# Kernel optimization log

Hardware: AMD Instinct MI355X
Metric: run time of the kernel (lower is better)

## Reference

```python
import jax, jax.numpy as jnp
import numpy as np

B, S, D = 2, 2048, 1024
H, DK, DV = 16, 64, 64
N_WINDOW = 256
LN_EPS = 1e-5


def setup_inputs() -> dict:
    key = jax.random.key(0)
    ks = jax.random.split(key, 8)
    sc = 0.02
    return {
        "Q": jax.random.normal(ks[0], (B, S, D), jnp.float32),
        "K": jax.random.normal(ks[1], (B, S, D), jnp.float32),
        "V": jax.random.normal(ks[2], (B, S, D), jnp.float32),
        "Wq": jax.random.normal(ks[3], (D, H * DK), jnp.float32) * sc,
        "bq": jnp.zeros((H * DK,), jnp.float32),
        "Wk": jax.random.normal(ks[4], (D, H * DK), jnp.float32) * sc,
        "bk": jnp.zeros((H * DK,), jnp.float32),
        "Wv": jax.random.normal(ks[5], (D, H * DV), jnp.float32) * sc,
        "bv": jnp.zeros((H * DV,), jnp.float32),
        "Wo": jax.random.normal(ks[6], (H * DV, D), jnp.float32) * sc,
        "bo": jnp.zeros((D,), jnp.float32),
        "gamma": jnp.ones((D,), jnp.float32),
        "beta": jnp.zeros((D,), jnp.float32),
    }


def reference(Q, K, V, Wq, bq, Wk, bk, Wv, bv, Wo, bo, gamma, beta):
    b, s, _ = Q.shape
    # QKV projections -> [b, s, h, d]
    q = (Q @ Wq + bq).reshape(b, s, H, DK)
    k = (K @ Wk + bk).reshape(b, s, H, DK)
    v = (V @ Wv + bv).reshape(b, s, H, DV)
    # scores [b, h, i, j]
    scores = jnp.einsum("bihd,bjhd->bhij", q, k) / np.sqrt(DK).astype(np.float32)
    # sliding-window band mask |i - j| < N_WINDOW (mask=True path)
    idx = jnp.arange(s)
    band = jnp.abs(idx[:, None] - idx[None, :]) < N_WINDOW  # [s, s]
    scores = jnp.where(band[None, None], scores, -jnp.inf)
    attn = jax.nn.softmax(scores, axis=-1)
    ctx = jnp.einsum("bhij,bjhd->bihd", attn, v).reshape(b, s, H * DV)
    out = ctx @ Wo + bo
    # residual + LayerNorm over last dim
    x = out + Q
    mu = jnp.mean(x, axis=-1, keepdims=True)
    var = jnp.mean(jnp.square(x - mu), axis=-1, keepdims=True)
    y = (x - mu) * jax.lax.rsqrt(var + LN_EPS) * gamma + beta
    return y, attn
```

## Files before the change

### kernel.cpp

```cpp
#include <hip/hip_runtime.h>
#include <hip/hip_bf16.h>

#define BB 2
#define SS 2048
#define HH 16
#define LN_EPS 1e-5f
#define LOG2E 1.44269504088896f

typedef __attribute__((ext_vector_type(8))) short short8;
typedef __attribute__((ext_vector_type(4))) float floatx4;

#define EXP2F(x) __builtin_amdgcn_exp2f(x)
#define GLOAD16(g, l) __builtin_amdgcn_global_load_lds( \
    (const __attribute__((address_space(1))) void*)(g), \
    (__attribute__((address_space(3))) void*)(l), 16, 0, 0)

__device__ __forceinline__ ushort f2b(float f) {
    union { float f; unsigned u; } x; x.f = f;
    unsigned u = x.u;
    return (ushort)((u + 0x7FFFu + ((u >> 16) & 1u)) >> 16);
}
__device__ __forceinline__ float b2f(ushort u) {
    union { unsigned u; float f; } x; x.u = ((unsigned)u) << 16;
    return x.f;
}

__global__ __launch_bounds__(256) void prep(
    const float* __restrict__ Q, const float* __restrict__ K, const float* __restrict__ V,
    const float* __restrict__ W0, const float* __restrict__ W1,
    const float* __restrict__ W2, const float* __restrict__ W3,
    ushort* __restrict__ Xq, ushort* __restrict__ Xk, ushort* __restrict__ Xv,
    ushort* __restrict__ T0, ushort* __restrict__ T1,
    ushort* __restrict__ T2, ushort* __restrict__ T3)
{
    __shared__ float ts[32][33];
    const int z = blockIdx.z;
    if (z < 3) {
        const float* X = z == 0 ? Q : z == 1 ? K : V;
        ushort* Y = z == 0 ? Xq : z == 1 ? Xk : Xv;
        const size_t i = ((size_t)blockIdx.x * 256 + threadIdx.x) * 8;
        float4 a = *(const float4*)&X[i];
        float4 b = *(const float4*)&X[i + 4];
        short8 o;
        o[0] = (short)f2b(a.x); o[1] = (short)f2b(a.y); o[2] = (short)f2b(a.z); o[3] = (short)f2b(a.w);
        o[4] = (short)f2b(b.x); o[5] = (short)f2b(b.y); o[6] = (short)f2b(b.z); o[7] = (short)f2b(b.w);
        *(short8*)&Y[i] = o;
    } else {
        if (blockIdx.x >= 1024) return;
        const int zz = z - 3;
        const float* W = zz == 0 ? W0 : zz == 1 ? W1 : zz == 2 ? W2 : W3;
        ushort* T = zz == 0 ? T0 : zz == 1 ? T1 : zz == 2 ? T2 : T3;
        const float scale = (zz == 0) ? 0.125f : 1.0f;
        const int k0 = (blockIdx.x >> 5) * 32, n0 = (blockIdx.x & 31) * 32;
        const int r = threadIdx.x >> 3, c4 = (threadIdx.x & 7) * 4;
        float4 v = *(const float4*)&W[(size_t)(k0 + r) * 1024 + n0 + c4];
        ts[r][c4 + 0] = v.x; ts[r][c4 + 1] = v.y; ts[r][c4 + 2] = v.z; ts[r][c4 + 3] = v.w;
        __syncthreads();
        ushort4 o;
        o.x = f2b(ts[c4 + 0][r] * scale); o.y = f2b(ts[c4 + 1][r] * scale);
        o.z = f2b(ts[c4 + 2][r] * scale); o.w = f2b(ts[c4 + 3][r] * scale);
        *(ushort4*)&T[(size_t)(n0 + r) * 1024 + k0 + c4] = o;
    }
}

template<int NB>
__device__ __forceinline__ void gemm_body(
    const ushort* __restrict__ Ab, const ushort* __restrict__ Bt,
    const float* __restrict__ bias, float bscale,
    float* Cf, ushort* Cb, int m0, int n0)
{
    __shared__ ushort As[2][128 * 32];
    __shared__ ushort Bs[2][NB * 32 * 32];
    const int t = threadIdx.x;
    const int l = t & 63;
    const int w = t >> 6;
    const int wm = w >> 1, wn = w & 1;

    floatx4 acc[4][NB] = {};

    const int i0c = w * 64 + l;
    const int r0 = i0c >> 2, c0 = i0c & 3;
    const int i1c = 256 + i0c;
    const int r1 = i1c >> 2, c1 = i1c & 3;

    const ushort* gA0 = &Ab[(size_t)(m0 + r0) * 1024 + c0 * 8];
    const ushort* gA1 = &Ab[(size_t)(m0 + r1) * 1024 + c1 * 8];
    const ushort* gB0 = &Bt[(size_t)(n0 + r0) * 1024 + c0 * 8];
    const ushort* gB1 = &Bt[(size_t)(n0 + ((NB == 4) ? r1 : r0)) * 1024 + ((NB == 4) ? c1 : c0) * 8];

    const int d0 = (w * 64) * 16;
    const int d1 = (256 + w * 64) * 16;

    GLOAD16(gA0, (char*)As[0] + d0);
    GLOAD16(gA1, (char*)As[0] + d1);
    GLOAD16(gB0, (char*)Bs[0] + d0);
    if (NB == 4) GLOAD16(gB1, (char*)Bs[0] + d1);
    __syncthreads();

    int cur = 0;
    for (int k0 = 0; k0 < 1024; k0 += 32) {
        if (k0 + 32 < 1024) {
            GLOAD16(gA0 + k0 + 32, (char*)As[cur ^ 1] + d0);
            GLOAD16(gA1 + k0 + 32, (char*)As[cur ^ 1] + d1);
            GLOAD16(gB0 + k0 + 32, (char*)Bs[cur ^ 1] + d0);
            if (NB == 4) GLOAD16(gB1 + k0 + 32, (char*)Bs[cur ^ 1] + d1);
        }
        short8 af[4], bf[NB];
#pragma unroll
        for (int m = 0; m < 4; ++m)
            af[m] = *(const short8*)&As[cur][(wm * 64 + m * 16 + (l & 15)) * 32 + (l >> 4) * 8];
#pragma unroll
        for (int n = 0; n < NB; ++n)
            bf[n] = *(const short8*)&Bs[cur][(wn * (NB * 16) + n * 16 + (l & 15)) * 32 + (l >> 4) * 8];
#pragma unroll
        for (int m = 0; m < 4; ++m)
#pragma unroll
            for (int n = 0; n < NB; ++n)
                acc[m][n] = __builtin_amdgcn_mfma_f32_16x16x32_bf16(af[m], bf[n], acc[m][n], 0, 0, 0);
        __syncthreads();
        cur ^= 1;
    }

    const int cr = (l >> 4) * 4;
    const int cc = l & 15;
#pragma unroll
    for (int n = 0; n < NB; ++n) {
        int col = n0 + wn * (NB * 16) + n * 16 + cc;
        float bv = bias[col] * bscale;
#pragma unroll
        for (int m = 0; m < 4; ++m) {
            int row = m0 + wm * 64 + m * 16 + cr;
#pragma unroll
            for (int j = 0; j < 4; ++j) {
                float v = acc[m][n][j] + bv;
                if (Cf) Cf[(size_t)(row + j) * 1024 + col] = v;
                else    Cb[(size_t)(row + j) * 1024 + col] = f2b(v);
            }
        }
    }
}

__global__ __launch_bounds__(256) void gemm_qkv(
    const ushort* __restrict__ Xq, const ushort* __restrict__ Xk, const ushort* __restrict__ Xv,
    const ushort* __restrict__ Wqt, const ushort* __restrict__ Wkt, const ushort* __restrict__ Wvt,
    const float* __restrict__ bq, const float* __restrict__ bk, const float* __restrict__ bv,
    ushort* __restrict__ qp, ushort* __restrict__ kp, ushort* __restrict__ vp)
{
    const int z = blockIdx.z;
    const ushort* A = z == 0 ? Xq : z == 1 ? Xk : Xv;
    const ushort* Bt = z == 0 ? Wqt : z == 1 ? Wkt : Wvt;
    const float* bias = z == 0 ? bq : z == 1 ? bk : bv;
    ushort* C = z == 0 ? qp : z == 1 ? kp : vp;
    float bscale = (z == 0) ? 0.125f : 1.0f;
    int bid = blockIdx.x + (blockIdx.y << 3);
    int xcd = bid & 7, idx = bid >> 3;
    int m0 = (xcd * 4 + (idx & 3)) * 128;
    int n0 = (idx >> 2) * 128;
    gemm_body<4>(A, Bt, bias, bscale, nullptr, C, m0, n0);
}

__global__ __launch_bounds__(256) void gemm_obf(
    const ushort* __restrict__ ctxb, const ushort* __restrict__ Wot,
    const float* __restrict__ bo, float* __restrict__ op)
{
    int bid = blockIdx.x + (blockIdx.y << 3);
    int xcd = bid & 7, idx = bid >> 3;
    int m0 = (xcd * 4 + (idx & 3)) * 128;
    int n0 = (idx >> 2) * 64;
    gemm_body<2>(ctxb, Wot, bo, 1.0f, op, nullptr, m0, n0);
}

__global__ __launch_bounds__(256, 4) void attn_mfma(
    const ushort* __restrict__ qb, const ushort* __restrict__ kb, const ushort* __restrict__ vb,
    float* __restrict__ attn, ushort* __restrict__ ctxb)
{
    __shared__ alignas(16) ushort Vt[2][64 * 72];
    __shared__ alignas(16) ushort Pl[4][16 * 72];

    const int qblk = blockIdx.x, h = blockIdx.y, b = blockIdx.z;
    const int i0 = qblk * 64;
    const int t = threadIdx.x;
    const int w = t >> 6, l = t & 63;
    const int g = l >> 4, c = l & 15;
    const int ibase = i0 + w * 16;

    const int jstart = max(0, i0 - 256);
    const int jend = min(SS, i0 + 64 + 256);

    const size_t qoff = (size_t)(b * SS + ibase + c) * 1024 + h * 64 + g * 8;
    short8 aq0 = *(const short8*)&qb[qoff];
    short8 aq1 = *(const short8*)&qb[qoff + 32];

    {
        float* ab = attn + (size_t)(b * HH + h) * SS * SS;
        const floatx4 z4 = {0.f, 0.f, 0.f, 0.f};
        const int g16 = t >> 4, c16 = t & 15;
#pragma unroll
        for (int rr = 0; rr < 4; ++rr) {
            float* rp = ab + (size_t)(i0 + g16 + rr * 16) * SS;
            for (int x = c16 * 4; x < jstart; x += 64)
                __builtin_nontemporal_store(z4, (floatx4*)&rp[x]);
            for (int x = jend + c16 * 4; x < SS; x += 64)
                __builtin_nontemporal_store(z4, (floatx4*)&rp[x]);
        }
    }

    const int vj0 = (t & 31) * 2, vd0 = (t >> 5) * 8;
    const ushort* Kbh = &kb[(size_t)(b * SS) * 1024 + h * 64];

    float m[4] = {-3e38f, -3e38f, -3e38f, -3e38f};
    float ll[4] = {0.f, 0.f, 0.f, 0.f};

    for (int jt = jstart; jt < jend; jt += 64) {
        const ushort* kt = Kbh + (size_t)jt * 1024;
        floatx4 s[4] = {};
#pragma unroll
        for (int u = 0; u < 4; ++u) {
            short8 b0 = *(const short8*)&kt[(size_t)(u * 16 + c) * 1024 + g * 8];
            short8 b1 = *(const short8*)&kt[(size_t)(u * 16 + c) * 1024 + 32 + g * 8];
            s[u] = __builtin_amdgcn_mfma_f32_16x16x32_bf16(aq0, b0, s[u], 0, 0, 0);
            s[u] = __builtin_amdgcn_mfma_f32_16x16x32_bf16(aq1, b1, s[u], 0, 0, 0);
        }
        const bool full = (jt >= ibase - 240) && (jt <= ibase + 192);
#pragma unroll
        for (int r = 0; r < 4; ++r) {
            float v0 = s[0][r] * LOG2E, v1 = s[1][r] * LOG2E,
                  v2 = s[2][r] * LOG2E, v3 = s[3][r] * LOG2E;
            if (!full) {
                const int i = ibase + g * 4 + r;
                const int j0 = jt + c;
                if ((unsigned)(i - j0 + 255) >= 511u)        v0 = -3e38f;
                if ((unsigned)(i - (j0 + 16) + 255) >= 511u) v1 = -3e38f;
                if ((unsigned)(i - (j0 + 32) + 255) >= 511u) v2 = -3e38f;
                if ((unsigned)(i - (j0 + 48) + 255) >= 511u) v3 = -3e38f;
            }
            float tmax = fmaxf(fmaxf(v0, v1), fmaxf(v2, v3));
            float mn = fmaxf(m[r], tmax);
            float sc_ = EXP2F(m[r] - mn);
            float add = EXP2F(v0 - mn) + EXP2F(v1 - mn)
                      + EXP2F(v2 - mn) + EXP2F(v3 - mn);
            ll[r] = ll[r] * sc_ + add;
            m[r] = mn;
        }
    }

    float M[4], invL[4];
#pragma unroll
    for (int r = 0; r < 4; ++r) {
        float mm = m[r];
        mm = fmaxf(mm, __shfl_xor(mm, 1));
        mm = fmaxf(mm, __shfl_xor(mm, 2));
        mm = fmaxf(mm, __shfl_xor(mm, 4));
        mm = fmaxf(mm, __shfl_xor(mm, 8));
        float la = ll[r] * EXP2F(m[r] - mm);
        la += __shfl_xor(la, 1);
        la += __shfl_xor(la, 2);
        la += __shfl_xor(la, 4);
        la += __shfl_xor(la, 8);
        M[r] = mm;
        invL[r] = 1.0f / la;
    }

    {
        const ushort* vr = &vb[(size_t)(b * SS + jstart + vj0) * 1024 + h * 64 + vd0];
        short8 v0 = *(const short8*)vr;
        short8 v1 = *(const short8*)(vr + 1024);
#pragma unroll
        for (int e = 0; e < 8; ++e) {
            ushort2 pr; pr.x = (ushort)v0[e]; pr.y = (ushort)v1[e];
            *(ushort2*)&Vt[0][(vd0 + e) * 72 + vj0] = pr;
        }
    }
    __syncthreads();

    floatx4 ctx[4] = {};
    int cur = 0;
    for (int jt = jstart; jt < jend; jt += 64) {
        const bool have = (jt + 64 < jend);
        short8 nv0, nv1;
        if (have) {
            const ushort* vr = &vb[(size_t)(b * SS + jt + 64 + vj0) * 1024 + h * 64 + vd0];
            nv0 = *(const short8*)vr;
            nv1 = *(const short8*)(vr + 1024);
        }
        const ushort* kt = Kbh + (size_t)jt * 1024;
        floatx4 s[4] = {};
#pragma unroll
        for (int u = 0; u < 4; ++u) {
            short8 b0 = *(const short8*)&kt[(size_t)(u * 16 + c) * 1024 + g * 8];
            short8 b1 = *(const short8*)&kt[(size_t)(u * 16 + c) * 1024 + 32 + g * 8];
            s[u] = __builtin_amdgcn_mfma_f32_16x16x32_bf16(aq0, b0, s[u], 0, 0, 0);
            s[u] = __builtin_amdgcn_mfma_f32_16x16x32_bf16(aq1, b1, s[u], 0, 0, 0);
        }
        const bool full = (jt >= ibase - 240) && (jt <= ibase + 192);
#pragma unroll
        for (int u = 0; u < 4; ++u) {
#pragma unroll
            for (int r = 0; r < 4; ++r) {
                float v = s[u][r] * LOG2E;
                if (!full) {
                    const int i = ibase + g * 4 + r;
                    const int j = jt + u * 16 + c;
                    if ((unsigned)(i - j + 255) >= 511u) v = -3e38f;
                }
                float p = EXP2F(v - M[r]) * invL[r];
                Pl[w][(g * 4 + r) * 72 + u * 16 + c] = f2b(p);
            }
        }
#pragma unroll
        for (int it = 0; it < 4; ++it) {
            const int row = it * 4 + g;
            ushort4 pw = *(const ushort4*)&Pl[w][row * 72 + c * 4];
            floatx4 o;
            o[0] = b2f(pw.x); o[1] = b2f(pw.y); o[2] = b2f(pw.z); o[3] = b2f(pw.w);
            __builtin_nontemporal_store(o,
                (floatx4*)&attn[(size_t)(b * HH + h) * SS * SS + (size_t)(ibase + row) * SS + jt + c * 4]);
        }
#pragma unroll
        for (int jc = 0; jc < 2; ++jc) {
            short8 pa = *(const short8*)&Pl[w][c * 72 + jc * 32 + g * 8];
#pragma unroll
            for (int ds = 0; ds < 4; ++ds) {
                short8 bv_ = *(const short8*)&Vt[cur][(ds * 16 + c) * 72 + jc * 32 + g * 8];
                ctx[ds] = __builtin_amdgcn_mfma_f32_16x16x32_bf16(pa, bv_, ctx[ds], 0, 0, 0);
            }
        }
        if (have) {
#pragma unroll
            for (int e = 0; e < 8; ++e) {
                ushort2 pr; pr.x = (ushort)nv0[e]; pr.y = (ushort)nv1[e];
                *(ushort2*)&Vt[cur ^ 1][(vd0 + e) * 72 + vj0] = pr;
            }
        }
        __syncthreads();
        cur ^= 1;
    }

#pragma unroll
    for (int ds = 0; ds < 4; ++ds)
#pragma unroll
        for (int r = 0; r < 4; ++r)
            ctxb[(size_t)(b * SS + ibase + g * 4 + r) * 1024 + h * 64 + ds * 16 + c] = f2b(ctx[ds][r]);
}

__global__ __launch_bounds__(256) void ln_kernel(
    const float* __restrict__ op, const float* __restrict__ Qin,
    const float* __restrict__ gamma, const float* __restrict__ beta,
    float* __restrict__ y)
{
    const int row = blockIdx.x;
    const int t = threadIdx.x;
    __shared__ float rs[4], rss[4];

    float4 o4 = *(const float4*)&op[(size_t)row * 1024 + t * 4];
    float4 q4 = *(const float4*)&Qin[(size_t)row * 1024 + t * 4];
    float x0 = o4.x + q4.x, x1 = o4.y + q4.y, x2 = o4.z + q4.z, x3 = o4.w + q4.w;
    float s = x0 + x1 + x2 + x3;
    float ss = x0 * x0 + x1 * x1 + x2 * x2 + x3 * x3;
#pragma unroll
    for (int off = 1; off < 64; off <<= 1) {
        s  += __shfl_xor(s, off, 64);
        ss += __shfl_xor(ss, off, 64);
    }
    int wid = t >> 6;
    if ((t & 63) == 0) { rs[wid] = s; rss[wid] = ss; }
    __syncthreads();
    s  = rs[0] + rs[1] + rs[2] + rs[3];
    ss = rss[0] + rss[1] + rss[2] + rss[3];
    float mu = s * (1.0f / 1024.0f);
    float var = ss * (1.0f / 1024.0f) - mu * mu;
    float rstd = rsqrtf(var + LN_EPS);
    float4 g4 = *(const float4*)&gamma[t * 4];
    float4 b4 = *(const float4*)&beta[t * 4];
    float4 o;
    o.x = (x0 - mu) * rstd * g4.x + b4.x;
    o.y = (x1 - mu) * rstd * g4.y + b4.y;
    o.z = (x2 - mu) * rstd * g4.z + b4.z;
    o.w = (x3 - mu) * rstd * g4.w + b4.w;
    *(float4*)&y[(size_t)row * 1024 + t * 4] = o;
}

extern "C" void kernel_launch(void* const* d_in, const int* in_sizes, int n_in,
                              void* d_out, int out_size, void* d_ws, size_t ws_size,
                              hipStream_t stream) {
    (void)in_sizes; (void)n_in; (void)out_size; (void)ws_size;
    const float* Q  = (const float*)d_in[0];
    const float* K  = (const float*)d_in[1];
    const float* V  = (const float*)d_in[2];
    const float* Wq = (const float*)d_in[3];
    const float* bq = (const float*)d_in[4];
    const float* Wk = (const float*)d_in[5];
    const float* bk = (const float*)d_in[6];
    const float* Wv = (const float*)d_in[7];
    const float* bv = (const float*)d_in[8];
    const float* Wo = (const float*)d_in[9];
    const float* bo = (const float*)d_in[10];
    const float* gamma = (const float*)d_in[11];
    const float* beta  = (const float*)d_in[12];

    float* y = (float*)d_out;
    float* attn = y + (size_t)BB * SS * 1024;

    char* base = (char*)d_ws;
    float*  op   = (float*)base;
    ushort* Xq   = (ushort*)base;
    ushort* Xk   = (ushort*)(base + (size_t)8 * 1048576);
    ushort* Xv   = (ushort*)(base + (size_t)16 * 1048576);
    ushort* ctxb = (ushort*)(base + (size_t)16 * 1048576);
    ushort* qbp  = (ushort*)(base + (size_t)24 * 1048576);
    ushort* kbp  = (ushort*)(base + (size_t)32 * 1048576);
    ushort* vbp  = (ushort*)(base + (size_t)40 * 1048576);
    ushort* Wqt  = (ushort*)(base + (size_t)48 * 1048576);
    ushort* Wkt  = (ushort*)(base + (size_t)50 * 1048576);
    ushort* Wvt  = (ushort*)(base + (size_t)52 * 1048576);
    ushort* Wot  = (ushort*)(base + (size_t)54 * 1048576);

    prep<<<dim3(2048, 1, 7), 256, 0, stream>>>(Q, K, V, Wq, Wk, Wv, Wo,
                                               Xq, Xk, Xv, Wqt, Wkt, Wvt, Wot);
    gemm_qkv<<<dim3(8, 32, 3), 256, 0, stream>>>(Xq, Xk, Xv, Wqt, Wkt, Wvt, bq, bk, bv, qbp, kbp, vbp);
    attn_mfma<<<dim3(SS / 64, HH, BB), 256, 0, stream>>>(qbp, kbp, vbp, attn, ctxb);
    gemm_obf<<<dim3(8, 64), 256, 0, stream>>>(ctxb, Wot, bo, op);
    ln_kernel<<<4096, 256, 0, stream>>>(op, Q, gamma, beta, y);
}
```

Measured before the change: 225.9 us.

## Overlap attention zero-fill stores with QKV and output GEMM main loops

Moves the zeroing of the out-of-band parts of the attention matrix out of the attention kernel and spreads it across the k-loop iterations of the QKV and output-projection GEMMs. Each GEMM block writes one 64x64 zero tile per iteration. The goal is to hide the large store traffic behind compute-bound MFMA work. The cost is extra bookkeeping and stores competing with the GEMM loads, plus a fixed tile enumeration that depends on exact grid sizes.

```diff
diff --git a/kernel.cpp b/kernel.cpp
--- a/kernel.cpp
+++ b/kernel.cpp
@@ -67,7 +67,8 @@
 __device__ __forceinline__ void gemm_body(
     const ushort* __restrict__ Ab, const ushort* __restrict__ Bt,
     const float* __restrict__ bias, float bscale,
-    float* Cf, ushort* Cb, int m0, int n0)
+    float* Cf, ushort* Cb, int m0, int n0,
+    float* __restrict__ attnf, int f_lo, int f_hi)
 {
     __shared__ ushort As[2][128 * 32];
     __shared__ ushort Bs[2][NB * 32 * 32];
@@ -90,6 +91,21 @@
 
     const int d0 = (w * 64) * 16;
     const int d1 = (256 + w * 64) * 16;
+
+    int fleft = f_hi - f_lo;
+    int fbh = 0, fq = 0, frr = 0;
+    if (fleft > 0) {
+        fbh = f_lo / 756;
+        int r = f_lo - fbh * 756;
+        while (true) {
+            int cnt = (fq > 4 ? fq - 4 : 0) + (fq < 27 ? 27 - fq : 0);
+            if (r < cnt) break;
+            r -= cnt; ++fq;
+        }
+        frr = r;
+    }
+    const int ftrow = t >> 2, ftc = (t & 3) * 16;
+    const floatx4 fz = {0.f, 0.f, 0.f, 0.f};
 
     GLOAD16(gA0, (char*)As[0] + d0);
     GLOAD16(gA1, (char*)As[0] + d1);
@@ -105,6 +121,19 @@
             GLOAD16(gB0 + k0 + 32, (char*)Bs[cur ^ 1] + d0);
             if (NB == 4) GLOAD16(gB1 + k0 + 32, (char*)Bs[cur ^ 1] + d1);
         }
+        if (fleft > 0) {
+            int L = fq > 4 ? fq - 4 : 0;
+            int col = (frr < L) ? frr * 64 : (fq * 64 + 320 + (frr - L) * 64);
+            float* fp = attnf + (size_t)fbh * ((size_t)SS * SS)
+                      + (size_t)(fq * 64 + ftrow) * SS + col + ftc;
+            __builtin_nontemporal_store(fz, (floatx4*)fp);
+            __builtin_nontemporal_store(fz, (floatx4*)(fp + 4));
+            __builtin_nontemporal_store(fz, (floatx4*)(fp + 8));
+            __builtin_nontemporal_store(fz, (floatx4*)(fp + 12));
+            --fleft; ++frr;
+            int cnt = L + (fq < 27 ? 27 - fq : 0);
+            if (frr >= cnt) { frr = 0; ++fq; if (fq == 32) { fq = 0; ++fbh; } }
+        }
         short8 af[4], bf[NB];
 #pragma unroll
         for (int m = 0; m < 4; ++m)
@@ -144,7 +173,8 @@
     const ushort* __restrict__ Xq, const ushort* __restrict__ Xk, const ushort* __restrict__ Xv,
     const ushort* __restrict__ Wqt, const ushort* __restrict__ Wkt, const ushort* __restrict__ Wvt,
     const float* __restrict__ bq, const float* __restrict__ bk, const float* __restrict__ bv,
-    ushort* __restrict__ qp, ushort* __restrict__ kp, ushort* __restrict__ vp)
+    ushort* __restrict__ qp, ushort* __restrict__ kp, ushort* __restrict__ vp,
+    float* __restrict__ attnf)
 {
     const int z = blockIdx.z;
     const ushort* A = z == 0 ? Xq : z == 1 ? Xk : Xv;
@@ -156,18 +186,22 @@
     int xcd = bid & 7, idx = bid >> 3;
     int m0 = (xcd * 4 + (idx & 3)) * 128;
     int n0 = (idx >> 2) * 128;
-    gemm_body<4>(A, Bt, bias, bscale, nullptr, C, m0, n0);
+    int k = bid + z * 256;
+    gemm_body<4>(A, Bt, bias, bscale, nullptr, C, m0, n0, attnf, k * 21, k * 21 + 21);
 }
 
 __global__ __launch_bounds__(256) void gemm_obf(
     const ushort* __restrict__ ctxb, const ushort* __restrict__ Wot,
-    const float* __restrict__ bo, float* __restrict__ op)
+    const float* __restrict__ bo, float* __restrict__ op,
+    float* __restrict__ attnf)
 {
     int bid = blockIdx.x + (blockIdx.y << 3);
     int xcd = bid & 7, idx = bid >> 3;
     int m0 = (xcd * 4 + (idx & 3)) * 128;
     int n0 = (idx >> 2) * 64;
-    gemm_body<2>(ctxb, Wot, bo, 1.0f, op, nullptr, m0, n0);
+    int lo = 16128 + bid * 16;
+    int hi = lo + 16; if (hi > 24192) hi = 24192; if (lo > 24192) lo = 24192;
+    gemm_body<2>(ctxb, Wot, bo, 1.0f, op, nullptr, m0, n0, attnf, lo, hi);
 }
 
 __global__ __launch_bounds__(256, 4) void attn_mfma(
@@ -190,20 +224,6 @@
     const size_t qoff = (size_t)(b * SS + ibase + c) * 1024 + h * 64 + g * 8;
     short8 aq0 = *(const short8*)&qb[qoff];
     short8 aq1 = *(const short8*)&qb[qoff + 32];
-
-    {
-        float* ab = attn + (size_t)(b * HH + h) * SS * SS;
-        const floatx4 z4 = {0.f, 0.f, 0.f, 0.f};
-        const int g16 = t >> 4, c16 = t & 15;
-#pragma unroll
-        for (int rr = 0; rr < 4; ++rr) {
-            float* rp = ab + (size_t)(i0 + g16 + rr * 16) * SS;
-            for (int x = c16 * 4; x < jstart; x += 64)
-                __builtin_nontemporal_store(z4, (floatx4*)&rp[x]);
-            for (int x = jend + c16 * 4; x < SS; x += 64)
-                __builtin_nontemporal_store(z4, (floatx4*)&rp[x]);
-        }
-    }
 
     const int vj0 = (t & 31) * 2, vd0 = (t >> 5) * 8;
     const ushort* Kbh = &kb[(size_t)(b * SS) * 1024 + h * 64];
@@ -417,8 +437,9 @@
 
     prep<<<dim3(2048, 1, 7), 256, 0, stream>>>(Q, K, V, Wq, Wk, Wv, Wo,
                                                Xq, Xk, Xv, Wqt, Wkt, Wvt, Wot);
-    gemm_qkv<<<dim3(8, 32, 3), 256, 0, stream>>>(Xq, Xk, Xv, Wqt, Wkt, Wvt, bq, bk, bv, qbp, kbp, vbp);
+    gemm_qkv<<<dim3(8, 32, 3), 256, 0, stream>>>(Xq, Xk, Xv, Wqt, Wkt, Wvt, bq, bk, bv,
+                                                 qbp, kbp, vbp, attn);
     attn_mfma<<<dim3(SS / 64, HH, BB), 256, 0, stream>>>(qbp, kbp, vbp, attn, ctxb);
-    gemm_obf<<<dim3(8, 64), 256, 0, stream>>>(ctxb, Wot, bo, op);
+    gemm_obf<<<dim3(8, 64), 256, 0, stream>>>(ctxb, Wot, bo, op, attn);
     ln_kernel<<<4096, 256, 0, stream>>>(op, Q, gamma, beta, y);
 }
```

Result: slower. 624.0 us (+176.2%).
